# Optimization experiments

Hardware: AMD Instinct MI355X
Metric: run time of the kernel (lower is better)

Reference implementation:

```python
import jax, jax.numpy as jnp
import numpy as np

D_MODEL = 1024
N_HEADS = 16
D_HEAD = 64


def setup_inputs() -> dict:
    key = jax.random.key(0)
    ks = jax.random.split(key, 5)
    B, T = 2, 2048
    scale = 1.0 / np.sqrt(D_MODEL)
    x = jax.random.normal(ks[0], (B, T, D_MODEL), dtype=jnp.float32)
    Wq = jax.random.normal(ks[1], (N_HEADS * D_HEAD, D_MODEL), dtype=jnp.float32) * scale
    Wk = jax.random.normal(ks[2], (N_HEADS * D_HEAD, D_MODEL), dtype=jnp.float32) * scale
    Wv = jax.random.normal(ks[3], (N_HEADS * D_HEAD, D_MODEL), dtype=jnp.float32) * scale
    Wo = jax.random.normal(ks[4], (D_MODEL, N_HEADS * D_HEAD), dtype=jnp.float32) * scale
    return {"x": x, "Wq": Wq, "Wk": Wk, "Wv": Wv, "Wo": Wo}


def reference(x, Wq, Wk, Wv, Wo):
    B, T, D = x.shape
    # Linear(y = x @ W.T), then split heads: [B, H, T, d]
    def split_heads(y):
        return y.reshape(B, T, N_HEADS, D_HEAD).transpose(0, 2, 1, 3)
    q = split_heads(x @ Wq.T)
    k = split_heads(x @ Wk.T)
    v = split_heads(x @ Wv.T)
    scale = D_HEAD ** -0.5
    # Materialized [B, H, T, T] scores, as in the original module
    scores = jnp.einsum('bhtd,bhTd->bhtT', q, k) * scale
    attn = jax.nn.softmax(scores, axis=-1)
    y = jnp.einsum('bhtT,bhTd->bhtd', attn, v)
    y = y.transpose(0, 2, 1, 3).reshape(B, T, N_HEADS * D_HEAD)
    return y @ Wo.T
```

## Files before the change

### kernel.cpp

```cpp
#include <hip/hip_runtime.h>
#include <hip/hip_bf16.h>

typedef __attribute__((ext_vector_type(8))) short bf16x8;
typedef __attribute__((ext_vector_type(4))) float f32x4;
typedef unsigned short u16t;

#define DEVINL static __device__ __forceinline__

DEVINL u16t f2bf(float f) {
  union { __hip_bfloat16 h; u16t u; } cv;
  cv.h = __float2bfloat16(f);
  return cv.u;
}

DEVINL void async16(void* lds, const void* g) {
  __builtin_amdgcn_global_load_lds((const __attribute__((address_space(1))) void*)g,
                                   (__attribute__((address_space(3))) void*)lds,
                                   16, 0, 0);
}

__global__ __launch_bounds__(256) void convert_bf16(
    const float* __restrict__ x,  const float* __restrict__ wq,
    const float* __restrict__ wk, const float* __restrict__ wv,
    const float* __restrict__ wo,
    u16t* __restrict__ xb, u16t* __restrict__ wqb, u16t* __restrict__ wkb,
    u16t* __restrict__ wvb, u16t* __restrict__ wob) {
  const int blk = blockIdx.x;
  const float* src; u16t* dst; size_t off;
  if (blk < 4096)      { src = x;  dst = xb;  off = (size_t)blk * 1024; }
  else if (blk < 5120) { src = wq; dst = wqb; off = (size_t)(blk - 4096) * 1024; }
  else if (blk < 6144) { src = wk; dst = wkb; off = (size_t)(blk - 5120) * 1024; }
  else if (blk < 7168) { src = wv; dst = wvb; off = (size_t)(blk - 6144) * 1024; }
  else                 { src = wo; dst = wob; off = (size_t)(blk - 7168) * 1024; }
  const size_t i = off + (size_t)threadIdx.x * 4;
  const float4 v = *(const float4*)&src[i];
  ushort4 r;
  r.x = f2bf(v.x); r.y = f2bf(v.y); r.z = f2bf(v.z); r.w = f2bf(v.w);
  *(ushort4*)&dst[i] = r;
}

template <int MODE>
__global__ __launch_bounds__(256) void gemm_bt(
    const u16t* __restrict__ A,
    const u16t* __restrict__ B0, const u16t* __restrict__ B1, const u16t* __restrict__ B2,
    void* __restrict__ C0, void* __restrict__ C1, void* __restrict__ C2,
    int M, int N, int K) {
  __shared__ u16t As[128 * 32];
  __shared__ u16t Bs[128 * 32];

  const u16t* B = B0;
  void* C = C0;
  if (blockIdx.z == 1) { B = B1; C = C1; }
  else if (blockIdx.z == 2) { B = B2; C = C2; }

  const int tid = threadIdx.x;
  const int lane = tid & 63;
  const int w = tid >> 6;
  const int wm = w >> 1, wn = w & 1;
  const int quad = lane >> 4, cl = lane & 15;
  const int m0 = blockIdx.y * 128;
  const int n0 = blockIdx.x * 128;

  const int srow = lane >> 2;
  const int scol = (lane & 3) * 8;

  f32x4 acc[4][4] = {};

  for (int k0 = 0; k0 < K; k0 += 32) {
    __syncthreads();
    #pragma unroll
    for (int ii = 0; ii < 2; ++ii) {
      const int c = w + ii * 4;
      async16(&As[c * 512], &A[(size_t)(m0 + c * 16 + srow) * K + k0 + scol]);
      async16(&Bs[c * 512], &B[(size_t)(n0 + c * 16 + srow) * K + k0 + scol]);
    }
    __syncthreads();
    bf16x8 af[4], bfr[4];
    #pragma unroll
    for (int i = 0; i < 4; ++i)
      af[i] = *(const bf16x8*)&As[(wm * 64 + i * 16 + cl) * 32 + quad * 8];
    #pragma unroll
    for (int j = 0; j < 4; ++j)
      bfr[j] = *(const bf16x8*)&Bs[(wn * 64 + j * 16 + cl) * 32 + quad * 8];
    #pragma unroll
    for (int i = 0; i < 4; ++i)
      #pragma unroll
      for (int j = 0; j < 4; ++j)
        acc[i][j] = __builtin_amdgcn_mfma_f32_16x16x32_bf16(af[i], bfr[j], acc[i][j], 0, 0, 0);
  }

  #pragma unroll
  for (int i = 0; i < 4; ++i)
    #pragma unroll
    for (int j = 0; j < 4; ++j) {
      const int mb = m0 + wm * 64 + i * 16 + quad * 4;
      const int n  = n0 + wn * 64 + j * 16 + cl;
      if (MODE == 1 && blockIdx.z == 2) {
        const int b = mb >> 11, tb = mb & 2047, h = n >> 6, d = n & 63;
        ushort4 v4;
        v4.x = f2bf(acc[i][j][0]); v4.y = f2bf(acc[i][j][1]);
        v4.z = f2bf(acc[i][j][2]); v4.w = f2bf(acc[i][j][3]);
        const size_t addr = ((size_t)(b * 16 + h) << 17) +
            (size_t)(((d >> 4) * 256 + (tb >> 3)) * 128 + (d & 15) * 8 + (tb & 7));
        *(ushort4*)&((u16t*)C)[addr] = v4;
      } else if (MODE == 1 && blockIdx.z == 1) {
        const int b = mb >> 11, tb = mb & 2047, h = n >> 6, d = n & 63;
        const size_t basea = ((size_t)(b * 16 + h) << 17) +
            (size_t)(((tb >> 4) * 8 + (d >> 3)) * 128 + (d & 7));
        #pragma unroll
        for (int r = 0; r < 4; ++r)
          ((u16t*)C)[basea + ((tb & 15) + r) * 8] = f2bf(acc[i][j][r]);
      } else {
        #pragma unroll
        for (int r = 0; r < 4; ++r) {
          const int m = mb + r;
          if (MODE == 0) {
            ((float*)C)[(size_t)m * N + n] = acc[i][j][r];
          } else {
            const int b = m >> 11, t = m & 2047, h = n >> 6, d = n & 63;
            ((u16t*)C)[(((size_t)(b * 16 + h)) * 2048 + t) * 64 + d] = f2bf(acc[i][j][r]);
          }
        }
      }
    }
}

__global__ __launch_bounds__(256) void flash_attn(
    const u16t* __restrict__ Q, const u16t* __restrict__ Kt,
    const u16t* __restrict__ Vt, u16t* __restrict__ Y) {
  __shared__ u16t Ps[4 * 16 * 136];

  const int tid = threadIdx.x;
  const int lane = tid & 63;
  const int w = tid >> 6;
  const int quad = lane >> 4, cl = lane & 15;
  const int bh = blockIdx.y;
  const int q0 = blockIdx.x * 64;
  const u16t* Kb = Kt + ((size_t)bh << 17);
  const u16t* Vb = Vt + ((size_t)bh << 17);

  bf16x8 aq[2];
  #pragma unroll
  for (int ks = 0; ks < 2; ++ks)
    aq[ks] = *(const bf16x8*)&Q[((size_t)bh * 2048 + q0 + w * 16 + cl) * 64 + ks * 32 + quad * 8];

  f32x4 o[4] = {};
  float lsum[4] = {0.f, 0.f, 0.f, 0.f};

  u16t* Pw = &Ps[w * 16 * 136];

  for (int jt = 0; jt < 16; ++jt) {
    const int j0 = jt * 128;

    f32x4 s[8] = {};
    #pragma unroll
    for (int ks = 0; ks < 2; ++ks) {
      bf16x8 kf[8];
      #pragma unroll
      for (int js = 0; js < 8; ++js)
        kf[js] = *(const bf16x8*)&Kb[(size_t)((((j0 >> 4) + js) * 8 + ks * 4) * 128) + lane * 8];
      #pragma unroll
      for (int js = 0; js < 8; ++js)
        s[js] = __builtin_amdgcn_mfma_f32_16x16x32_bf16(aq[ks], kf[js], s[js], 0, 0, 0);
    }

    #pragma unroll
    for (int js = 0; js < 8; ++js)
      #pragma unroll
      for (int r = 0; r < 4; ++r) {
        const float p = __builtin_exp2f(s[js][r] * 0.1803368801111593f);
        lsum[r] += p;
        Pw[(quad * 4 + r) * 136 + js * 16 + cl] = f2bf(p);
      }

    #pragma unroll
    for (int ks = 0; ks < 4; ++ks) {
      const bf16x8 ap = *(const bf16x8*)&Pw[cl * 136 + ks * 32 + quad * 8];
      bf16x8 vf[4];
      #pragma unroll
      for (int ds = 0; ds < 4; ++ds)
        vf[ds] = *(const bf16x8*)&Vb[(size_t)((ds * 256 + (j0 >> 3) + ks * 4) * 128) + lane * 8];
      #pragma unroll
      for (int ds = 0; ds < 4; ++ds)
        o[ds] = __builtin_amdgcn_mfma_f32_16x16x32_bf16(ap, vf[ds], o[ds], 0, 0, 0);
    }
  }

  #pragma unroll
  for (int r = 0; r < 4; ++r) {
    #pragma unroll
    for (int msk = 1; msk < 16; msk <<= 1) lsum[r] += __shfl_xor(lsum[r], msk, 64);
  }

  const int b = bh >> 4, h = bh & 15;
  #pragma unroll
  for (int ds = 0; ds < 4; ++ds)
    #pragma unroll
    for (int r = 0; r < 4; ++r) {
      const int t = q0 + w * 16 + quad * 4 + r;
      const int d = ds * 16 + cl;
      Y[((size_t)b * 2048 + t) * 1024 + h * 64 + d] = f2bf(o[ds][r] / lsum[r]);
    }
}

extern "C" void kernel_launch(void* const* d_in, const int* in_sizes, int n_in,
                              void* d_out, int out_size, void* d_ws, size_t ws_size,
                              hipStream_t stream) {
  (void)in_sizes; (void)n_in; (void)out_size; (void)ws_size;
  const float* x  = (const float*)d_in[0];
  const float* Wq = (const float*)d_in[1];
  const float* Wk = (const float*)d_in[2];
  const float* Wv = (const float*)d_in[3];
  const float* Wo = (const float*)d_in[4];

  char* ws = (char*)d_ws;
  const size_t MB = 1024 * 1024;
  u16t* xb  = (u16t*)(ws);
  u16t* Wqb = (u16t*)(ws + 8 * MB);
  u16t* Wkb = (u16t*)(ws + 10 * MB);
  u16t* Wvb = (u16t*)(ws + 12 * MB);
  u16t* Wob = (u16t*)(ws + 14 * MB);
  u16t* Qw  = (u16t*)(ws + 16 * MB);
  u16t* Ktw = (u16t*)(ws + 24 * MB);
  u16t* Vtw = (u16t*)(ws + 32 * MB);
  u16t* Yw  = xb;

  convert_bf16<<<8192, 256, 0, stream>>>(x, Wq, Wk, Wv, Wo, xb, Wqb, Wkb, Wvb, Wob);
  gemm_bt<1><<<dim3(8, 32, 3), 256, 0, stream>>>(
      xb, Wqb, Wkb, Wvb, Qw, Ktw, Vtw, 4096, 1024, 1024);
  flash_attn<<<dim3(32, 32), 256, 0, stream>>>(Qw, Ktw, Vtw, Yw);
  gemm_bt<0><<<dim3(8, 32, 1), 256, 0, stream>>>(
      Yw, Wob, Wob, Wob, d_out, d_out, d_out, 4096, 1024, 1024);
}
```

Before: 221.3 us.

## Split attention KV loop across wave groups and merge QKV into one GEMM

The attention kernel now runs 512 threads per block. Two groups of four waves each handle half of the key/value tiles for the same query rows, and their partial outputs and row sums are combined through LDS before normalisation, giving more in-flight waves and shorter per-wave loops. The QKV projection becomes a single GEMM with N=3072, relying on Wq, Wk and Wv sitting contiguously in the workspace, and the output layout is chosen from the column index instead of blockIdx.z. The GEMM main loop stages 64 K elements per barrier pair instead of 32, halving synchronisation at the cost of double the LDS per block.

```diff
diff --git a/kernel.cpp b/kernel.cpp
--- a/kernel.cpp
+++ b/kernel.cpp
@@ -41,17 +41,11 @@
 
 template <int MODE>
 __global__ __launch_bounds__(256) void gemm_bt(
-    const u16t* __restrict__ A,
-    const u16t* __restrict__ B0, const u16t* __restrict__ B1, const u16t* __restrict__ B2,
+    const u16t* __restrict__ A, const u16t* __restrict__ B,
     void* __restrict__ C0, void* __restrict__ C1, void* __restrict__ C2,
     int M, int N, int K) {
-  __shared__ u16t As[128 * 32];
-  __shared__ u16t Bs[128 * 32];
-
-  const u16t* B = B0;
-  void* C = C0;
-  if (blockIdx.z == 1) { B = B1; C = C1; }
-  else if (blockIdx.z == 2) { B = B2; C = C2; }
+  __shared__ u16t As[2][128 * 32];
+  __shared__ u16t Bs[2][128 * 32];
 
   const int tid = threadIdx.x;
   const int lane = tid & 63;
@@ -66,73 +60,81 @@
 
   f32x4 acc[4][4] = {};
 
-  for (int k0 = 0; k0 < K; k0 += 32) {
+  for (int k0 = 0; k0 < K; k0 += 64) {
     __syncthreads();
     #pragma unroll
-    for (int ii = 0; ii < 2; ++ii) {
-      const int c = w + ii * 4;
-      async16(&As[c * 512], &A[(size_t)(m0 + c * 16 + srow) * K + k0 + scol]);
-      async16(&Bs[c * 512], &B[(size_t)(n0 + c * 16 + srow) * K + k0 + scol]);
-    }
+    for (int p = 0; p < 2; ++p)
+      #pragma unroll
+      for (int ii = 0; ii < 2; ++ii) {
+        const int c = w + ii * 4;
+        async16(&As[p][c * 512], &A[(size_t)(m0 + c * 16 + srow) * K + k0 + p * 32 + scol]);
+        async16(&Bs[p][c * 512], &B[(size_t)(n0 + c * 16 + srow) * K + k0 + p * 32 + scol]);
+      }
     __syncthreads();
-    bf16x8 af[4], bfr[4];
-    #pragma unroll
-    for (int i = 0; i < 4; ++i)
-      af[i] = *(const bf16x8*)&As[(wm * 64 + i * 16 + cl) * 32 + quad * 8];
-    #pragma unroll
-    for (int j = 0; j < 4; ++j)
-      bfr[j] = *(const bf16x8*)&Bs[(wn * 64 + j * 16 + cl) * 32 + quad * 8];
-    #pragma unroll
-    for (int i = 0; i < 4; ++i)
+    #pragma unroll
+    for (int p = 0; p < 2; ++p) {
+      bf16x8 af[4], bfr[4];
+      #pragma unroll
+      for (int i = 0; i < 4; ++i)
+        af[i] = *(const bf16x8*)&As[p][(wm * 64 + i * 16 + cl) * 32 + quad * 8];
       #pragma unroll
       for (int j = 0; j < 4; ++j)
-        acc[i][j] = __builtin_amdgcn_mfma_f32_16x16x32_bf16(af[i], bfr[j], acc[i][j], 0, 0, 0);
-  }
-
+        bfr[j] = *(const bf16x8*)&Bs[p][(wn * 64 + j * 16 + cl) * 32 + quad * 8];
+      #pragma unroll
+      for (int i = 0; i < 4; ++i)
+        #pragma unroll
+        for (int j = 0; j < 4; ++j)
+          acc[i][j] = __builtin_amdgcn_mfma_f32_16x16x32_bf16(af[i], bfr[j], acc[i][j], 0, 0, 0);
+    }
+  }
+
+  const int nz = n0 >> 10;
   #pragma unroll
   for (int i = 0; i < 4; ++i)
     #pragma unroll
     for (int j = 0; j < 4; ++j) {
       const int mb = m0 + wm * 64 + i * 16 + quad * 4;
       const int n  = n0 + wn * 64 + j * 16 + cl;
-      if (MODE == 1 && blockIdx.z == 2) {
-        const int b = mb >> 11, tb = mb & 2047, h = n >> 6, d = n & 63;
-        ushort4 v4;
-        v4.x = f2bf(acc[i][j][0]); v4.y = f2bf(acc[i][j][1]);
-        v4.z = f2bf(acc[i][j][2]); v4.w = f2bf(acc[i][j][3]);
-        const size_t addr = ((size_t)(b * 16 + h) << 17) +
-            (size_t)(((d >> 4) * 256 + (tb >> 3)) * 128 + (d & 15) * 8 + (tb & 7));
-        *(ushort4*)&((u16t*)C)[addr] = v4;
-      } else if (MODE == 1 && blockIdx.z == 1) {
-        const int b = mb >> 11, tb = mb & 2047, h = n >> 6, d = n & 63;
-        const size_t basea = ((size_t)(b * 16 + h) << 17) +
-            (size_t)(((tb >> 4) * 8 + (d >> 3)) * 128 + (d & 7));
+      if (MODE == 0) {
         #pragma unroll
         for (int r = 0; r < 4; ++r)
-          ((u16t*)C)[basea + ((tb & 15) + r) * 8] = f2bf(acc[i][j][r]);
+          ((float*)C0)[(size_t)(mb + r) * N + n] = acc[i][j][r];
       } else {
-        #pragma unroll
-        for (int r = 0; r < 4; ++r) {
-          const int m = mb + r;
-          if (MODE == 0) {
-            ((float*)C)[(size_t)m * N + n] = acc[i][j][r];
-          } else {
-            const int b = m >> 11, t = m & 2047, h = n >> 6, d = n & 63;
-            ((u16t*)C)[(((size_t)(b * 16 + h)) * 2048 + t) * 64 + d] = f2bf(acc[i][j][r]);
-          }
+        const int nw = n & 1023, h = nw >> 6, d = nw & 63;
+        const int b = mb >> 11, tb = mb & 2047;
+        const size_t bh = (size_t)(b * 16 + h);
+        if (nz == 2) {
+          ushort4 v4;
+          v4.x = f2bf(acc[i][j][0]); v4.y = f2bf(acc[i][j][1]);
+          v4.z = f2bf(acc[i][j][2]); v4.w = f2bf(acc[i][j][3]);
+          const size_t addr = (bh << 17) +
+              (size_t)(((d >> 4) * 256 + (tb >> 3)) * 128 + (d & 15) * 8 + (tb & 7));
+          *(ushort4*)&((u16t*)C2)[addr] = v4;
+        } else if (nz == 1) {
+          const size_t basea = (bh << 17) +
+              (size_t)(((tb >> 4) * 8 + (d >> 3)) * 128 + (d & 7));
+          #pragma unroll
+          for (int r = 0; r < 4; ++r)
+            ((u16t*)C1)[basea + ((tb & 15) + r) * 8] = f2bf(acc[i][j][r]);
+        } else {
+          #pragma unroll
+          for (int r = 0; r < 4; ++r)
+            ((u16t*)C0)[(bh * 2048 + tb + r) * 64 + d] = f2bf(acc[i][j][r]);
         }
       }
     }
 }
 
-__global__ __launch_bounds__(256) void flash_attn(
+__global__ __launch_bounds__(512) void flash_attn(
     const u16t* __restrict__ Q, const u16t* __restrict__ Kt,
     const u16t* __restrict__ Vt, u16t* __restrict__ Y) {
-  __shared__ u16t Ps[4 * 16 * 136];
+  __shared__ u16t Ps[8 * 16 * 136];
 
   const int tid = threadIdx.x;
   const int lane = tid & 63;
   const int w = tid >> 6;
+  const int wq = w & 3;
+  const int kh = w >> 2;
   const int quad = lane >> 4, cl = lane & 15;
   const int bh = blockIdx.y;
   const int q0 = blockIdx.x * 64;
@@ -142,14 +144,14 @@
   bf16x8 aq[2];
   #pragma unroll
   for (int ks = 0; ks < 2; ++ks)
-    aq[ks] = *(const bf16x8*)&Q[((size_t)bh * 2048 + q0 + w * 16 + cl) * 64 + ks * 32 + quad * 8];
+    aq[ks] = *(const bf16x8*)&Q[((size_t)bh * 2048 + q0 + wq * 16 + cl) * 64 + ks * 32 + quad * 8];
 
   f32x4 o[4] = {};
   float lsum[4] = {0.f, 0.f, 0.f, 0.f};
 
   u16t* Pw = &Ps[w * 16 * 136];
 
-  for (int jt = 0; jt < 16; ++jt) {
+  for (int jt = kh * 8; jt < kh * 8 + 8; ++jt) {
     const int j0 = jt * 128;
 
     f32x4 s[8] = {};
@@ -186,21 +188,40 @@
     }
   }
 
-  #pragma unroll
-  for (int r = 0; r < 4; ++r) {
-    #pragma unroll
-    for (int msk = 1; msk < 16; msk <<= 1) lsum[r] += __shfl_xor(lsum[r], msk, 64);
-  }
-
-  const int b = bh >> 4, h = bh & 15;
-  #pragma unroll
-  for (int ds = 0; ds < 4; ++ds)
+  __syncthreads();
+  float* M = (float*)Ps;
+  if (kh == 1) {
+    float* slot = &M[((size_t)((w - 4) * 64 + lane)) * 21];
+    #pragma unroll
+    for (int ds = 0; ds < 4; ++ds)
+      #pragma unroll
+      for (int r = 0; r < 4; ++r) slot[ds * 4 + r] = o[ds][r];
+    #pragma unroll
+    for (int r = 0; r < 4; ++r) slot[16 + r] = lsum[r];
+  }
+  __syncthreads();
+  if (kh == 0) {
+    const float* slot = &M[((size_t)(w * 64 + lane)) * 21];
+    #pragma unroll
+    for (int ds = 0; ds < 4; ++ds)
+      #pragma unroll
+      for (int r = 0; r < 4; ++r) o[ds][r] += slot[ds * 4 + r];
     #pragma unroll
     for (int r = 0; r < 4; ++r) {
-      const int t = q0 + w * 16 + quad * 4 + r;
-      const int d = ds * 16 + cl;
-      Y[((size_t)b * 2048 + t) * 1024 + h * 64 + d] = f2bf(o[ds][r] / lsum[r]);
-    }
+      lsum[r] += slot[16 + r];
+      #pragma unroll
+      for (int msk = 1; msk < 16; msk <<= 1) lsum[r] += __shfl_xor(lsum[r], msk, 64);
+    }
+    const int b = bh >> 4, h = bh & 15;
+    #pragma unroll
+    for (int ds = 0; ds < 4; ++ds)
+      #pragma unroll
+      for (int r = 0; r < 4; ++r) {
+        const int t = q0 + wq * 16 + quad * 4 + r;
+        const int d = ds * 16 + cl;
+        Y[((size_t)b * 2048 + t) * 1024 + h * 64 + d] = f2bf(o[ds][r] / lsum[r]);
+      }
+  }
 }
 
 extern "C" void kernel_launch(void* const* d_in, const int* in_sizes, int n_in,
@@ -226,9 +247,9 @@
   u16t* Yw  = xb;
 
   convert_bf16<<<8192, 256, 0, stream>>>(x, Wq, Wk, Wv, Wo, xb, Wqb, Wkb, Wvb, Wob);
-  gemm_bt<1><<<dim3(8, 32, 3), 256, 0, stream>>>(
-      xb, Wqb, Wkb, Wvb, Qw, Ktw, Vtw, 4096, 1024, 1024);
-  flash_attn<<<dim3(32, 32), 256, 0, stream>>>(Qw, Ktw, Vtw, Yw);
-  gemm_bt<0><<<dim3(8, 32, 1), 256, 0, stream>>>(
-      Yw, Wob, Wob, Wob, d_out, d_out, d_out, 4096, 1024, 1024);
-}
+  gemm_bt<1><<<dim3(24, 32), 256, 0, stream>>>(
+      xb, Wqb, Qw, Ktw, Vtw, 4096, 3072, 1024);
+  flash_attn<<<dim3(32, 32), 512, 0, stream>>>(Qw, Ktw, Vtw, Yw);
+  gemm_bt<0><<<dim3(8, 32), 256, 0, stream>>>(
+      Yw, Wob, d_out, d_out, d_out, 4096, 1024, 1024);
+}
```

Measured after the change: 224.9 us. About the same (+1.6%).
